# Kernel tuning notes

Hardware: AMD Instinct MI355X
Metric: run time of the kernel (lower is better)

Reference implementation:

```python
import jax, jax.numpy as jnp
import numpy as np

B, N, F = 8, 1024, 256
H, U = 4, 256
NEG = -1e9  # unused (adjacency=None -> full attention)


def setup_inputs() -> dict:
    key = jax.random.key(0)
    k1, k2, k3, k4 = jax.random.split(key, 4)
    x = jax.random.normal(k1, (B, N, F), dtype=jnp.float32)
    # glorot-scale params
    W = jax.random.normal(k2, (H, F, U), dtype=jnp.float32) * (2.0 / (F + U)) ** 0.5
    a_src = jax.random.normal(k3, (H, U, 1), dtype=jnp.float32) * (2.0 / (U + 1)) ** 0.5
    a_dst = jax.random.normal(k4, (H, U, 1), dtype=jnp.float32) * (2.0 / (U + 1)) ** 0.5
    return {"x": x, "W": W, "a_src": a_src, "a_dst": a_dst}


def reference(x, W, a_src, a_dst):
    # per-head linear projection: [B,H,N,U]
    h = jnp.einsum('bnf,hfu->bhnu', x, W)
    # additive attention logits
    src = jnp.einsum('bhnu,hu->bhn', h, a_src[..., 0])  # [B,H,N]
    dst = jnp.einsum('bhnu,hu->bhn', h, a_dst[..., 0])  # [B,H,N]
    scores = src[:, :, :, None] + dst[:, :, None, :]    # [B,H,N,N]
    scores = jax.nn.leaky_relu(scores, negative_slope=0.2)
    attn = jax.nn.softmax(scores, axis=-1)
    h_prime = jnp.einsum('bhnm,bhmu->bhnu', attn, h)    # [B,H,N,U]
    # concat heads: [B,N,H*U]
    return jnp.transpose(h_prime, (0, 2, 1, 3)).reshape(B, N, H * U)
```

## Files before the change

kernel.cpp:

```cpp
#include <hip/hip_runtime.h>
#include <math.h>

constexpr int B_ = 8, N_ = 1024, F_ = 256, H_ = 4, U_ = 256;
constexpr int BH_ = B_ * H_;
constexpr int CH_ = 16;
constexpr int NCH_ = N_ / CH_;
constexpr int M_ = B_ * N_;

typedef short short8 __attribute__((ext_vector_type(8)));
typedef float floatx4 __attribute__((ext_vector_type(4)));

__device__ inline unsigned short f2bf(float f) {
    unsigned u = __float_as_uint(f);
    u += 0x7fff + ((u >> 16) & 1);
    return (unsigned short)(u >> 16);
}
__device__ inline float bf2f(unsigned short s) { return __uint_as_float(((unsigned)s) << 16); }

__device__ inline void gload_lds16(const void* g, void* l) {
    __builtin_amdgcn_global_load_lds(
        (const __attribute__((address_space(1))) void*)g,
        (__attribute__((address_space(3))) void*)(unsigned)(uintptr_t)l,
        16, 0, 0);
}

__global__ __launch_bounds__(256) void prep_w(const float* __restrict__ W,
                                              const float* __restrict__ asr,
                                              const float* __restrict__ ads,
                                              unsigned short* __restrict__ whT,
                                              float* __restrict__ c_src,
                                              float* __restrict__ c_dst) {
    int tid = threadIdx.x;
    if (blockIdx.x < 64) {
        __shared__ float t[64][65];
        int bi = blockIdx.x;
        int f0 = (bi & 3) * 64, u0 = ((bi >> 2) & 3) * 64, h = bi >> 4;
        int c = tid & 63, rbase = tid >> 6;
        #pragma unroll
        for (int rr = 0; rr < 16; ++rr) {
            int r = rr * 4 + rbase;
            t[r][c] = W[((size_t)(h * F_ + f0 + r)) * U_ + u0 + c];
        }
        __syncthreads();
        #pragma unroll
        for (int rr = 0; rr < 16; ++rr) {
            int r = rr * 4 + rbase;
            whT[((size_t)(h * U_ + u0 + r)) * F_ + f0 + c] = f2bf(t[c][r]);
        }
    } else {
        int id = blockIdx.x - 64;
        int h = id >> 2, f0 = (id & 3) * 64;
        int fl = tid >> 2, q = tid & 3;
        int f = f0 + fl;
        const float* Wrow = W + ((size_t)(h * F_ + f)) * U_ + q * 64;
        const float* av = asr + h * U_ + q * 64;
        const float* bv = ads + h * U_ + q * 64;
        float s = 0.f, d = 0.f;
        #pragma unroll
        for (int u = 0; u < 64; ++u) { float ww = Wrow[u]; s += ww * av[u]; d += ww * bv[u]; }
        s += __shfl_xor(s, 1); s += __shfl_xor(s, 2);
        d += __shfl_xor(d, 1); d += __shfl_xor(d, 2);
        if (q == 0) { c_src[h * F_ + f] = s; c_dst[h * F_ + f] = d; }
    }
}

__global__ __launch_bounds__(256) void k1b_fused(const float* __restrict__ x,
                                                 const float* __restrict__ c_src,
                                                 const float* __restrict__ c_dst,
                                                 unsigned short* __restrict__ xh,
                                                 float* __restrict__ srcv,
                                                 float* __restrict__ dstv) {
    int tid = threadIdx.x;
    int lane = tid & 63, w = tid >> 6;
    int row = blockIdx.x * 4 + w;
    int b = row >> 10, n = row & 1023;
    const float4 x4 = *(const float4*)(x + (size_t)row * F_ + lane * 4);
    ushort4 hv;
    hv.x = f2bf(x4.x); hv.y = f2bf(x4.y); hv.z = f2bf(x4.z); hv.w = f2bf(x4.w);
    ((ushort4*)xh)[(size_t)row * (F_ / 4) + lane] = hv;
    #pragma unroll
    for (int hh = 0; hh < H_; ++hh) {
        float4 c4 = *(const float4*)(c_src + hh * F_ + lane * 4);
        float s = x4.x*c4.x + x4.y*c4.y + x4.z*c4.z + x4.w*c4.w;
        #pragma unroll
        for (int off = 32; off; off >>= 1) s += __shfl_xor(s, off);
        float4 d4 = *(const float4*)(c_dst + hh * F_ + lane * 4);
        float d = x4.x*d4.x + x4.y*d4.y + x4.z*d4.z + x4.w*d4.w;
        #pragma unroll
        for (int off = 32; off; off >>= 1) d += __shfl_xor(d, off);
        if (lane == 0) {
            srcv[(size_t)(b * H_ + hh) * N_ + n] = s;
            dstv[(size_t)(b * H_ + hh) * N_ + n] = d;
        }
    }
}

__global__ __launch_bounds__(1024) void k2_all(const float* __restrict__ dstv,
                                               const float* __restrict__ srcv,
                                               float* __restrict__ dvs,
                                               int* __restrict__ invp,
                                               int* __restrict__ spos,
                                               int* __restrict__ srows,
                                               float* __restrict__ se8,
                                               int* __restrict__ cstart) {
    __shared__ float dv[N_];
    __shared__ float keyLA[N_]; __shared__ int idxLA[N_];
    __shared__ float keyLB[N_]; __shared__ int idxLB[N_];
    int bh = blockIdx.x, t = threadIdx.x;

    float ka = dstv[(size_t)bh * N_ + t];  int ia = t;
    float kb = -srcv[(size_t)bh * N_ + t]; int ib = t;

    for (int k = 2; k <= N_; k <<= 1) {
        for (int j = k >> 1; j > 0; j >>= 1) {
            bool up = ((t & k) == 0);
            bool lower = ((t & j) == 0);
            float oa, ob; int oia, oib;
            if (j >= 64) {
                keyLA[t] = ka; idxLA[t] = ia;
                keyLB[t] = kb; idxLB[t] = ib;
                __syncthreads();
                oa = keyLA[t ^ j]; oia = idxLA[t ^ j];
                ob = keyLB[t ^ j]; oib = idxLB[t ^ j];
                __syncthreads();
            } else {
                oa = __shfl_xor(ka, j); oia = __shfl_xor(ia, j);
                ob = __shfl_xor(kb, j); oib = __shfl_xor(ib, j);
            }
            bool swa = up ? (lower ? (ka > oa) : (ka < oa))
                          : (lower ? (ka < oa) : (ka > oa));
            if (swa) { ka = oa; ia = oia; }
            bool swb = up ? (lower ? (kb > ob) : (kb < ob))
                          : (lower ? (kb < ob) : (kb > ob));
            if (swb) { kb = ob; ib = oib; }
        }
    }

    dvs[(size_t)bh * N_ + t] = ka;
    invp[(size_t)bh * N_ + ia] = t;
    dv[t] = ka;
    __syncthreads();

    float s = -kb;
    int lo = 0, hi = N_;
    while (lo < hi) {
        int mid = (lo + hi) >> 1;
        if (dv[mid] <= kb) lo = mid + 1; else hi = mid;
    }
    spos[(size_t)bh * N_ + t] = lo;
    srows[(size_t)bh * N_ + t] = ib;
    se8[(size_t)bh * N_ + t] = expf(0.8f * s);
    idxLA[t] = lo;
    __syncthreads();
    if (t < NCH_ + 1) {
        int target = t * CH_;
        int lo2 = 0, hi2 = N_;
        while (lo2 < hi2) {
            int mid = (lo2 + hi2) >> 1;
            if (idxLA[mid] < target) lo2 = mid + 1; else hi2 = mid;
        }
        cstart[bh * (NCH_ + 1) + t] = lo2;
    }
}

__global__ __launch_bounds__(256) void k1_mfma(const unsigned short* __restrict__ xh,
                                               const unsigned short* __restrict__ whT,
                                               const int* __restrict__ invp,
                                               unsigned short* __restrict__ hbuf) {
    __shared__ __align__(16) unsigned short As[2 * 128 * 64];
    __shared__ int jsL[128];
    unsigned short* Bs = As + 128 * 64;
    const int tid = threadIdx.x;
    const int lane = tid & 63, wv = tid >> 6;
    const int wr = wv >> 1, wc = wv & 1;
    const int m0 = blockIdx.x * 128;
    const int u0 = blockIdx.y * 128;
    const int hh = blockIdx.z;
    const int b = m0 >> 10, n0 = m0 & 1023;
    const int bh = b * H_ + hh;

    floatx4 acc[4][4] = {};

    const char* Asrc = (const char*)xh;
    const char* Bsrc = (const char*)(whT + (size_t)hh * U_ * F_);

    const int ch_row = lane >> 3;
    const int ch_col = (lane & 7) * 16;

    for (int t = 0; t < 4; ++t) {
        const size_t kb = (size_t)t * 128;
        #pragma unroll
        for (int i = 0; i < 4; ++i) {
            int c = wv * 4 + i;
            int row = c * 8 + ch_row;
            gload_lds16(Asrc + (size_t)(m0 + row) * 512 + kb + ch_col,
                        (char*)As + c * 1024);
            gload_lds16(Bsrc + (size_t)(u0 + row) * 512 + kb + ch_col,
                        (char*)Bs + c * 1024);
        }
        __syncthreads();
        #pragma unroll
        for (int ks = 0; ks < 2; ++ks) {
            short8 af[4], bfr[4];
            #pragma unroll
            for (int mf = 0; mf < 4; ++mf) {
                int row = wr * 64 + mf * 16 + (lane & 15);
                af[mf] = *(const short8*)&As[row * 64 + ks * 32 + (lane >> 4) * 8];
            }
            #pragma unroll
            for (int nf = 0; nf < 4; ++nf) {
                int row = wc * 64 + nf * 16 + (lane & 15);
                bfr[nf] = *(const short8*)&Bs[row * 64 + ks * 32 + (lane >> 4) * 8];
            }
            #pragma unroll
            for (int mf = 0; mf < 4; ++mf)
                #pragma unroll
                for (int nf = 0; nf < 4; ++nf)
                    acc[mf][nf] = __builtin_amdgcn_mfma_f32_16x16x32_bf16(
                        af[mf], bfr[nf], acc[mf][nf], 0, 0, 0);
        }
        __syncthreads();
    }

    unsigned short* S = As;
    const int rquad = (lane >> 4) * 4;
    const int ucol = lane & 15;
    #pragma unroll
    for (int mf = 0; mf < 4; ++mf)
        #pragma unroll
        for (int j = 0; j < 4; ++j) {
            int rloc = wr * 64 + mf * 16 + rquad + j;
            #pragma unroll
            for (int nf = 0; nf < 4; ++nf)
                S[rloc * 128 + wc * 64 + nf * 16 + ucol] = f2bf(acc[mf][nf][j]);
        }
    if (tid < 128) jsL[tid] = invp[(size_t)bh * N_ + n0 + tid];
    __syncthreads();
    #pragma unroll
    for (int i = 0; i < 8; ++i) {
        int flat = tid + i * 256;
        int rloc = flat >> 4, slot = flat & 15;
        short8 v = *(const short8*)&S[rloc * 128 + slot * 8];
        *(short8*)&hbuf[((size_t)bh * N_ + jsL[rloc]) * U_ + u0 + slot * 8] = v;
    }
}

__global__ __launch_bounds__(256) void k3a_partial(const unsigned short* __restrict__ hbuf,
                                                   const float* __restrict__ dvs,
                                                   float* __restrict__ cT1, float* __restrict__ cT2,
                                                   float* __restrict__ cZ1, float* __restrict__ cZ2) {
    __shared__ float w1s[CH_], w2s[CH_];
    __shared__ floatx4 A1s[4][64], A2s[4][64];
    int bh = blockIdx.x / NCH_, c = blockIdx.x % NCH_;
    int tid = threadIdx.x, w = tid >> 6, l = tid & 63;
    const ushort4* hb4 = (const ushort4*)(hbuf + ((size_t)bh * N_ + c * CH_) * U_);
    ushort4 h0 = hb4[(4 * w + 0) * 64 + l];
    ushort4 h1 = hb4[(4 * w + 1) * 64 + l];
    ushort4 h2 = hb4[(4 * w + 2) * 64 + l];
    ushort4 h3 = hb4[(4 * w + 3) * 64 + l];
    floatx4 v0 = {bf2f(h0.x), bf2f(h0.y), bf2f(h0.z), bf2f(h0.w)};
    floatx4 v1 = {bf2f(h1.x), bf2f(h1.y), bf2f(h1.z), bf2f(h1.w)};
    floatx4 v2 = {bf2f(h2.x), bf2f(h2.y), bf2f(h2.z), bf2f(h2.w)};
    floatx4 v3 = {bf2f(h3.x), bf2f(h3.y), bf2f(h3.z), bf2f(h3.w)};
    if (tid < CH_) {
        float vv = dvs[(size_t)bh * N_ + c * CH_ + tid];
        w1s[tid] = expf(vv);
        w2s[tid] = expf(0.2f * vv);
    }
    __syncthreads();
    floatx4 s1 = w1s[4*w]*v0 + w1s[4*w+1]*v1 + w1s[4*w+2]*v2 + w1s[4*w+3]*v3;
    floatx4 s2 = w2s[4*w]*v0 + w2s[4*w+1]*v1 + w2s[4*w+2]*v2 + w2s[4*w+3]*v3;
    A1s[w][l] = s1; A2s[w][l] = s2;
    __syncthreads();
    if (tid < 64) {
        floatx4 r1 = A1s[0][tid] + A1s[1][tid] + A1s[2][tid] + A1s[3][tid];
        floatx4 r2 = A2s[0][tid] + A2s[1][tid] + A2s[2][tid] + A2s[3][tid];
        ((floatx4*)(cT1 + (size_t)(bh * NCH_ + c) * U_))[tid] = r1;
        ((floatx4*)(cT2 + (size_t)(bh * NCH_ + c) * U_))[tid] = r2;
    }
    if (tid == 0) {
        float z1 = 0.f, z2 = 0.f;
        #pragma unroll
        for (int r = 0; r < CH_; ++r) { z1 += w1s[r]; z2 += w2s[r]; }
        cZ1[bh * NCH_ + c] = z1; cZ2[bh * NCH_ + c] = z2;
    }
}

__global__ __launch_bounds__(256) void k3b_combine(const float* __restrict__ cT1, const float* __restrict__ cT2,
                                                   const float* __restrict__ cZ1, const float* __restrict__ cZ2,
                                                   float* __restrict__ b1, float* __restrict__ b2,
                                                   float* __restrict__ bz1, float* __restrict__ bz2) {
    int bh = blockIdx.x;
    int u = threadIdx.x;
    float v[NCH_];
    #pragma unroll
    for (int c = 0; c < NCH_; ++c) v[c] = cT2[(size_t)(bh * NCH_ + c) * U_ + u];
    float acc2 = 0.f;
    #pragma unroll
    for (int c = 0; c < NCH_; ++c) {
        b2[(size_t)(bh * NCH_ + c) * U_ + u] = acc2;
        acc2 += v[c];
    }
    #pragma unroll
    for (int c = 0; c < NCH_; ++c) v[c] = cT1[(size_t)(bh * NCH_ + c) * U_ + u];
    float acc1 = 0.f;
    #pragma unroll
    for (int c = NCH_ - 1; c >= 0; --c) {
        b1[(size_t)(bh * NCH_ + c) * U_ + u] = acc1;
        acc1 += v[c];
    }
    if (u < NCH_) {
        float z1 = cZ1[bh * NCH_ + u];
        float z2 = cZ2[bh * NCH_ + u];
        float i1 = z1, i2 = z2;
        #pragma unroll
        for (int off = 1; off < NCH_; off <<= 1) {
            float t1 = __shfl_up(i1, off, 64);
            float t2 = __shfl_up(i2, off, 64);
            if (u >= off) { i1 += t1; i2 += t2; }
        }
        float tot1 = __shfl(i1, NCH_ - 1, 64);
        bz1[bh * NCH_ + u] = tot1 - i1;
        bz2[bh * NCH_ + u] = i2 - z2;
    }
}

__global__ __launch_bounds__(256) void k3cd_emit(const unsigned short* __restrict__ hbuf,
                                                 const float* __restrict__ dvs,
                                                 const float* __restrict__ b1, const float* __restrict__ b2,
                                                 const float* __restrict__ bz1, const float* __restrict__ bz2,
                                                 const int* __restrict__ spos,
                                                 const int* __restrict__ srows,
                                                 const float* __restrict__ se8,
                                                 const int* __restrict__ cstart,
                                                 float* __restrict__ out) {
    __shared__ floatx4 P1s[CH_ + 1][64];
    __shared__ floatx4 P2s[CH_ + 1][64];
    __shared__ floatx4 T1s[4][64], T2s[4][64];
    __shared__ float w1s[CH_], w2s[CH_];
    __shared__ float zx1[CH_ + 1], zx2[CH_ + 1];
    __shared__ int sps[256], srs[256];
    __shared__ float s8s[256];

    int bh = blockIdx.x / NCH_, c = blockIdx.x % NCH_;
    int tid = threadIdx.x, w = tid >> 6, l = tid & 63;
    int b = bh >> 2, hh = bh & 3;

    const ushort4* hb4 = (const ushort4*)(hbuf + ((size_t)bh * N_ + c * CH_) * U_);
    ushort4 h0 = hb4[(4 * w + 0) * 64 + l];
    ushort4 h1 = hb4[(4 * w + 1) * 64 + l];
    ushort4 h2 = hb4[(4 * w + 2) * 64 + l];
    ushort4 h3 = hb4[(4 * w + 3) * 64 + l];
    floatx4 v0 = {bf2f(h0.x), bf2f(h0.y), bf2f(h0.z), bf2f(h0.w)};
    floatx4 v1 = {bf2f(h1.x), bf2f(h1.y), bf2f(h1.z), bf2f(h1.w)};
    floatx4 v2 = {bf2f(h2.x), bf2f(h2.y), bf2f(h2.z), bf2f(h2.w)};
    floatx4 v3 = {bf2f(h3.x), bf2f(h3.y), bf2f(h3.z), bf2f(h3.w)};
    if (tid < CH_) {
        float vv = dvs[(size_t)bh * N_ + c * CH_ + tid];
        w1s[tid] = expf(vv);
        w2s[tid] = expf(0.2f * vv);
    }
    __syncthreads();
    float a0 = w1s[4*w], a1 = w1s[4*w+1], a2 = w1s[4*w+2], a3 = w1s[4*w+3];
    float c0 = w2s[4*w], c1 = w2s[4*w+1], c2 = w2s[4*w+2], c3 = w2s[4*w+3];
    floatx4 q1_1 = a0 * v0;
    floatx4 q1_2 = q1_1 + a1 * v1;
    floatx4 q1_3 = q1_2 + a2 * v2;
    floatx4 tw1  = q1_3 + a3 * v3;
    floatx4 q2_1 = c0 * v0;
    floatx4 q2_2 = q2_1 + c1 * v1;
    floatx4 q2_3 = q2_2 + c2 * v2;
    floatx4 tw2  = q2_3 + c3 * v3;
    T1s[w][l] = tw1; T2s[w][l] = tw2;
    if (tid == 0) {
        float z1 = 0.f, z2 = 0.f;
        #pragma unroll
        for (int r = 0; r < CH_; ++r) { zx1[r] = z1; zx2[r] = z2; z1 += w1s[r]; z2 += w2s[r]; }
        zx1[CH_] = z1; zx2[CH_] = z2;
    }
    __syncthreads();
    floatx4 base1 = {0.f, 0.f, 0.f, 0.f}, base2 = {0.f, 0.f, 0.f, 0.f};
    if (w > 0) { base1 += T1s[0][l]; base2 += T2s[0][l]; }
    if (w > 1) { base1 += T1s[1][l]; base2 += T2s[1][l]; }
    if (w > 2) { base1 += T1s[2][l]; base2 += T2s[2][l]; }
    P1s[4*w+0][l] = base1;         P2s[4*w+0][l] = base2;
    P1s[4*w+1][l] = base1 + q1_1;  P2s[4*w+1][l] = base2 + q2_1;
    P1s[4*w+2][l] = base1 + q1_2;  P2s[4*w+2][l] = base2 + q2_2;
    P1s[4*w+3][l] = base1 + q1_3;  P2s[4*w+3][l] = base2 + q2_3;
    if (w == 3) { P1s[CH_][l] = base1 + tw1; P2s[CH_][l] = base2 + tw2; }
    __syncthreads();

    floatx4 t1 = P1s[CH_][l];
    float tz1 = zx1[CH_];
    floatx4 b1u = ((const floatx4*)(b1 + (size_t)(bh * NCH_ + c) * U_))[l];
    floatx4 b2u = ((const floatx4*)(b2 + (size_t)(bh * NCH_ + c) * U_))[l];
    float bz1c = bz1[bh * NCH_ + c], bz2c = bz2[bh * NCH_ + c];

    const int*   spos_b  = spos  + (size_t)bh * N_;
    const int*   srows_b = srows + (size_t)bh * N_;
    const float* se8_b   = se8   + (size_t)bh * N_;
    const int j0 = cstart[bh * (NCH_ + 1) + c];
    const int e0 = (c == NCH_ - 1) ? N_ : cstart[bh * (NCH_ + 1) + c + 1];

    for (int t0 = j0; t0 < e0; t0 += 256) {
        int jj = t0 + tid;
        if (jj < e0) { sps[tid] = spos_b[jj]; srs[tid] = srows_b[jj]; s8s[tid] = se8_b[jj]; }
        __syncthreads();
        int cnt = min(256, e0 - t0);
        for (int k = w; k < cnt; k += 4) {
            int   rr  = sps[k] - c * CH_;
            int   row = srs[k];
            float e8  = s8s[k];
            floatx4 s1 = b1u + (t1 - P1s[rr][l]);
            floatx4 s2 = b2u + P2s[rr][l];
            float den = e8 * (bz1c + (tz1 - zx1[rr])) + (bz2c + zx2[rr]);
            float rden = 1.0f / den;
            floatx4 o = (e8 * s1 + s2) * rden;
            *(floatx4*)(out + ((size_t)(b * N_ + row)) * (H_ * U_) + hh * U_ + 4 * l) = o;
        }
        __syncthreads();
    }
}

extern "C" void kernel_launch(void* const* d_in, const int* in_sizes, int n_in,
                              void* d_out, int out_size, void* d_ws, size_t ws_size,
                              hipStream_t stream) {
    const float* x    = (const float*)d_in[0];
    const float* W    = (const float*)d_in[1];
    const float* asr  = (const float*)d_in[2];
    const float* ads  = (const float*)d_in[3];
    float* out = (float*)d_out;

    char* ws = (char*)d_ws;
    size_t off = 0;
    auto alloc = [&](size_t nfloats) -> float* {
        float* p = (float*)(ws + off);
        off += ((nfloats * 4 + 255) / 256) * 256;
        return p;
    };
    unsigned short* hbuf = (unsigned short*)alloc((size_t)BH_ * N_ * U_ / 2);
    float* srcv  = alloc((size_t)BH_ * N_);
    float* dstv  = alloc((size_t)BH_ * N_);
    float* c_src = alloc(H_ * F_);
    float* c_dst = alloc(H_ * F_);
    float* dvs   = alloc((size_t)BH_ * N_);
    int*   invp  = (int*)alloc((size_t)BH_ * N_);
    int*   srows = (int*)alloc((size_t)BH_ * N_);
    int*   spos  = (int*)alloc((size_t)BH_ * N_);
    float* se8   = alloc((size_t)BH_ * N_);
    int*   cstart= (int*)alloc(BH_ * (NCH_ + 1));
    float* cT1   = alloc((size_t)BH_ * NCH_ * U_);
    float* cT2   = alloc((size_t)BH_ * NCH_ * U_);
    float* cZ1   = alloc(BH_ * NCH_);
    float* cZ2   = alloc(BH_ * NCH_);
    float* b1    = alloc((size_t)BH_ * NCH_ * U_);
    float* b2    = alloc((size_t)BH_ * NCH_ * U_);
    float* bz1   = alloc(BH_ * NCH_);
    float* bz2   = alloc(BH_ * NCH_);
    unsigned short* xh  = (unsigned short*)alloc((size_t)M_ * F_ / 2);
    unsigned short* whT = (unsigned short*)alloc((size_t)H_ * U_ * F_ / 2);
    (void)ws_size; (void)in_sizes; (void)n_in; (void)out_size;

    prep_w<<<80, 256, 0, stream>>>(W, asr, ads, whT, c_src, c_dst);
    k1b_fused<<<(B_ * N_) / 4, 256, 0, stream>>>(x, c_src, c_dst, xh, srcv, dstv);
    k2_all<<<BH_, 1024, 0, stream>>>(dstv, srcv, dvs, invp, spos, srows, se8, cstart);
    k1_mfma<<<dim3(M_ / 128, U_ / 128, H_), 256, 0, stream>>>(xh, whT, invp, hbuf);
    k3a_partial<<<BH_ * NCH_, 256, 0, stream>>>(hbuf, dvs, cT1, cT2, cZ1, cZ2);
    k3b_combine<<<BH_, 256, 0, stream>>>(cT1, cT2, cZ1, cZ2, b1, b2, bz1, bz2);
    k3cd_emit<<<BH_ * NCH_, 256, 0, stream>>>(hbuf, dvs, b1, b2, bz1, bz2,
                                              spos, srows, se8, cstart, out);
}
```

Measured before the change: 82.71 us.

## Fuse three-stage chunked prefix-scan attention into one per-head kernel

Replaces the partial-sum, combine and emit kernels (plus cstart computation in the sort kernel) with a single kernel where each block handles one batch-head and a 64-column slice. Eight segments of 128 rows compute segment totals, combine them through LDS, then rescan their rows while emitting outputs for the sorted source positions. This removes two launches and the global round-trips of per-chunk partial sums. The trade-off is far fewer blocks (128 of 512 threads), serial per-thread loops over 128 rows, scalar 2-byte loads, and possible load imbalance when many sources fall in one segment.

After: 114.0 us. 37.8% more time.

```diff
diff --git a/kernel.cpp b/kernel.cpp
--- a/kernel.cpp
+++ b/kernel.cpp
@@ -3,8 +3,6 @@
 
 constexpr int B_ = 8, N_ = 1024, F_ = 256, H_ = 4, U_ = 256;
 constexpr int BH_ = B_ * H_;
-constexpr int CH_ = 16;
-constexpr int NCH_ = N_ / CH_;
 constexpr int M_ = B_ * N_;
 
 typedef short short8 __attribute__((ext_vector_type(8)));
@@ -101,8 +99,7 @@
                                                int* __restrict__ invp,
                                                int* __restrict__ spos,
                                                int* __restrict__ srows,
-                                               float* __restrict__ se8,
-                                               int* __restrict__ cstart) {
+                                               float* __restrict__ se8) {
     __shared__ float dv[N_];
     __shared__ float keyLA[N_]; __shared__ int idxLA[N_];
     __shared__ float keyLB[N_]; __shared__ int idxLB[N_];
@@ -150,17 +147,6 @@
     spos[(size_t)bh * N_ + t] = lo;
     srows[(size_t)bh * N_ + t] = ib;
     se8[(size_t)bh * N_ + t] = expf(0.8f * s);
-    idxLA[t] = lo;
-    __syncthreads();
-    if (t < NCH_ + 1) {
-        int target = t * CH_;
-        int lo2 = 0, hi2 = N_;
-        while (lo2 < hi2) {
-            int mid = (lo2 + hi2) >> 1;
-            if (idxLA[mid] < target) lo2 = mid + 1; else hi2 = mid;
-        }
-        cstart[bh * (NCH_ + 1) + t] = lo2;
-    }
 }
 
 __global__ __launch_bounds__(256) void k1_mfma(const unsigned short* __restrict__ xh,
@@ -178,6 +164,8 @@
     const int hh = blockIdx.z;
     const int b = m0 >> 10, n0 = m0 & 1023;
     const int bh = b * H_ + hh;
+
+    if (tid < 128) jsL[tid] = invp[(size_t)bh * N_ + n0 + tid];
 
     floatx4 acc[4][4] = {};
 
@@ -234,7 +222,6 @@
             for (int nf = 0; nf < 4; ++nf)
                 S[rloc * 128 + wc * 64 + nf * 16 + ucol] = f2bf(acc[mf][nf][j]);
         }
-    if (tid < 128) jsL[tid] = invp[(size_t)bh * N_ + n0 + tid];
     __syncthreads();
     #pragma unroll
     for (int i = 0; i < 8; ++i) {
@@ -245,180 +232,110 @@
     }
 }
 
-__global__ __launch_bounds__(256) void k3a_partial(const unsigned short* __restrict__ hbuf,
-                                                   const float* __restrict__ dvs,
-                                                   float* __restrict__ cT1, float* __restrict__ cT2,
-                                                   float* __restrict__ cZ1, float* __restrict__ cZ2) {
-    __shared__ float w1s[CH_], w2s[CH_];
-    __shared__ floatx4 A1s[4][64], A2s[4][64];
-    int bh = blockIdx.x / NCH_, c = blockIdx.x % NCH_;
-    int tid = threadIdx.x, w = tid >> 6, l = tid & 63;
-    const ushort4* hb4 = (const ushort4*)(hbuf + ((size_t)bh * N_ + c * CH_) * U_);
-    ushort4 h0 = hb4[(4 * w + 0) * 64 + l];
-    ushort4 h1 = hb4[(4 * w + 1) * 64 + l];
-    ushort4 h2 = hb4[(4 * w + 2) * 64 + l];
-    ushort4 h3 = hb4[(4 * w + 3) * 64 + l];
-    floatx4 v0 = {bf2f(h0.x), bf2f(h0.y), bf2f(h0.z), bf2f(h0.w)};
-    floatx4 v1 = {bf2f(h1.x), bf2f(h1.y), bf2f(h1.z), bf2f(h1.w)};
-    floatx4 v2 = {bf2f(h2.x), bf2f(h2.y), bf2f(h2.z), bf2f(h2.w)};
-    floatx4 v3 = {bf2f(h3.x), bf2f(h3.y), bf2f(h3.z), bf2f(h3.w)};
-    if (tid < CH_) {
-        float vv = dvs[(size_t)bh * N_ + c * CH_ + tid];
-        w1s[tid] = expf(vv);
-        w2s[tid] = expf(0.2f * vv);
+__global__ __launch_bounds__(512) void k3_fused(const unsigned short* __restrict__ hbuf,
+                                                const float* __restrict__ dvs,
+                                                const int* __restrict__ spos,
+                                                const int* __restrict__ srows,
+                                                const float* __restrict__ se8,
+                                                float* __restrict__ out) {
+    __shared__ float w1s[N_], w2s[N_];
+    __shared__ int   sposL[N_], srowsL[N_];
+    __shared__ float se8L[N_];
+    __shared__ float t1L[8][64], t2L[8][64];
+    __shared__ float zt1L[8], zt2L[8];
+
+    const int blk = blockIdx.x;
+    const int bh = blk >> 2, slice = blk & 3;
+    const int tid = threadIdx.x;
+    const int lane = tid & 63, seg = tid >> 6;
+    const int b = bh >> 2, hh = bh & 3;
+
+    for (int i = tid; i < N_; i += 512) {
+        float vv = dvs[(size_t)bh * N_ + i];
+        w1s[i] = expf(vv);
+        w2s[i] = expf(0.2f * vv);
+        sposL[i]  = spos[(size_t)bh * N_ + i];
+        srowsL[i] = srows[(size_t)bh * N_ + i];
+        se8L[i]   = se8[(size_t)bh * N_ + i];
     }
     __syncthreads();
-    floatx4 s1 = w1s[4*w]*v0 + w1s[4*w+1]*v1 + w1s[4*w+2]*v2 + w1s[4*w+3]*v3;
-    floatx4 s2 = w2s[4*w]*v0 + w2s[4*w+1]*v1 + w2s[4*w+2]*v2 + w2s[4*w+3]*v3;
-    A1s[w][l] = s1; A2s[w][l] = s2;
+
+    const unsigned short* hbp =
+        hbuf + ((size_t)bh * N_ + seg * 128) * U_ + slice * 64 + lane;
+
+    float t1 = 0.f, t2 = 0.f;
+    #pragma unroll 16
+    for (int r = 0; r < 128; ++r) {
+        float v = bf2f(hbp[(size_t)r * U_]);
+        t1 += w1s[seg * 128 + r] * v;
+        t2 += w2s[seg * 128 + r] * v;
+    }
+    t1L[seg][lane] = t1; t2L[seg][lane] = t2;
+    float zz1 = 0.f, zz2 = 0.f;
+    for (int r = lane; r < 128; r += 64) {
+        zz1 += w1s[seg * 128 + r];
+        zz2 += w2s[seg * 128 + r];
+    }
+    #pragma unroll
+    for (int off = 32; off; off >>= 1) {
+        zz1 += __shfl_xor(zz1, off);
+        zz2 += __shfl_xor(zz2, off);
+    }
+    if (lane == 0) { zt1L[seg] = zz1; zt2L[seg] = zz2; }
     __syncthreads();
-    if (tid < 64) {
-        floatx4 r1 = A1s[0][tid] + A1s[1][tid] + A1s[2][tid] + A1s[3][tid];
-        floatx4 r2 = A2s[0][tid] + A2s[1][tid] + A2s[2][tid] + A2s[3][tid];
-        ((floatx4*)(cT1 + (size_t)(bh * NCH_ + c) * U_))[tid] = r1;
-        ((floatx4*)(cT2 + (size_t)(bh * NCH_ + c) * U_))[tid] = r2;
-    }
-    if (tid == 0) {
-        float z1 = 0.f, z2 = 0.f;
-        #pragma unroll
-        for (int r = 0; r < CH_; ++r) { z1 += w1s[r]; z2 += w2s[r]; }
-        cZ1[bh * NCH_ + c] = z1; cZ2[bh * NCH_ + c] = z2;
-    }
-}
-
-__global__ __launch_bounds__(256) void k3b_combine(const float* __restrict__ cT1, const float* __restrict__ cT2,
-                                                   const float* __restrict__ cZ1, const float* __restrict__ cZ2,
-                                                   float* __restrict__ b1, float* __restrict__ b2,
-                                                   float* __restrict__ bz1, float* __restrict__ bz2) {
-    int bh = blockIdx.x;
-    int u = threadIdx.x;
-    float v[NCH_];
-    #pragma unroll
-    for (int c = 0; c < NCH_; ++c) v[c] = cT2[(size_t)(bh * NCH_ + c) * U_ + u];
-    float acc2 = 0.f;
-    #pragma unroll
-    for (int c = 0; c < NCH_; ++c) {
-        b2[(size_t)(bh * NCH_ + c) * U_ + u] = acc2;
-        acc2 += v[c];
-    }
-    #pragma unroll
-    for (int c = 0; c < NCH_; ++c) v[c] = cT1[(size_t)(bh * NCH_ + c) * U_ + u];
-    float acc1 = 0.f;
-    #pragma unroll
-    for (int c = NCH_ - 1; c >= 0; --c) {
-        b1[(size_t)(bh * NCH_ + c) * U_ + u] = acc1;
-        acc1 += v[c];
-    }
-    if (u < NCH_) {
-        float z1 = cZ1[bh * NCH_ + u];
-        float z2 = cZ2[bh * NCH_ + u];
-        float i1 = z1, i2 = z2;
-        #pragma unroll
-        for (int off = 1; off < NCH_; off <<= 1) {
-            float t1 = __shfl_up(i1, off, 64);
-            float t2 = __shfl_up(i2, off, 64);
-            if (u >= off) { i1 += t1; i2 += t2; }
-        }
-        float tot1 = __shfl(i1, NCH_ - 1, 64);
-        bz1[bh * NCH_ + u] = tot1 - i1;
-        bz2[bh * NCH_ + u] = i2 - z2;
-    }
-}
-
-__global__ __launch_bounds__(256) void k3cd_emit(const unsigned short* __restrict__ hbuf,
-                                                 const float* __restrict__ dvs,
-                                                 const float* __restrict__ b1, const float* __restrict__ b2,
-                                                 const float* __restrict__ bz1, const float* __restrict__ bz2,
-                                                 const int* __restrict__ spos,
-                                                 const int* __restrict__ srows,
-                                                 const float* __restrict__ se8,
-                                                 const int* __restrict__ cstart,
-                                                 float* __restrict__ out) {
-    __shared__ floatx4 P1s[CH_ + 1][64];
-    __shared__ floatx4 P2s[CH_ + 1][64];
-    __shared__ floatx4 T1s[4][64], T2s[4][64];
-    __shared__ float w1s[CH_], w2s[CH_];
-    __shared__ float zx1[CH_ + 1], zx2[CH_ + 1];
-    __shared__ int sps[256], srs[256];
-    __shared__ float s8s[256];
-
-    int bh = blockIdx.x / NCH_, c = blockIdx.x % NCH_;
-    int tid = threadIdx.x, w = tid >> 6, l = tid & 63;
-    int b = bh >> 2, hh = bh & 3;
-
-    const ushort4* hb4 = (const ushort4*)(hbuf + ((size_t)bh * N_ + c * CH_) * U_);
-    ushort4 h0 = hb4[(4 * w + 0) * 64 + l];
-    ushort4 h1 = hb4[(4 * w + 1) * 64 + l];
-    ushort4 h2 = hb4[(4 * w + 2) * 64 + l];
-    ushort4 h3 = hb4[(4 * w + 3) * 64 + l];
-    floatx4 v0 = {bf2f(h0.x), bf2f(h0.y), bf2f(h0.z), bf2f(h0.w)};
-    floatx4 v1 = {bf2f(h1.x), bf2f(h1.y), bf2f(h1.z), bf2f(h1.w)};
-    floatx4 v2 = {bf2f(h2.x), bf2f(h2.y), bf2f(h2.z), bf2f(h2.w)};
-    floatx4 v3 = {bf2f(h3.x), bf2f(h3.y), bf2f(h3.z), bf2f(h3.w)};
-    if (tid < CH_) {
-        float vv = dvs[(size_t)bh * N_ + c * CH_ + tid];
-        w1s[tid] = expf(vv);
-        w2s[tid] = expf(0.2f * vv);
-    }
-    __syncthreads();
-    float a0 = w1s[4*w], a1 = w1s[4*w+1], a2 = w1s[4*w+2], a3 = w1s[4*w+3];
-    float c0 = w2s[4*w], c1 = w2s[4*w+1], c2 = w2s[4*w+2], c3 = w2s[4*w+3];
-    floatx4 q1_1 = a0 * v0;
-    floatx4 q1_2 = q1_1 + a1 * v1;
-    floatx4 q1_3 = q1_2 + a2 * v2;
-    floatx4 tw1  = q1_3 + a3 * v3;
-    floatx4 q2_1 = c0 * v0;
-    floatx4 q2_2 = q2_1 + c1 * v1;
-    floatx4 q2_3 = q2_2 + c2 * v2;
-    floatx4 tw2  = q2_3 + c3 * v3;
-    T1s[w][l] = tw1; T2s[w][l] = tw2;
-    if (tid == 0) {
-        float z1 = 0.f, z2 = 0.f;
-        #pragma unroll
-        for (int r = 0; r < CH_; ++r) { zx1[r] = z1; zx2[r] = z2; z1 += w1s[r]; z2 += w2s[r]; }
-        zx1[CH_] = z1; zx2[CH_] = z2;
-    }
-    __syncthreads();
-    floatx4 base1 = {0.f, 0.f, 0.f, 0.f}, base2 = {0.f, 0.f, 0.f, 0.f};
-    if (w > 0) { base1 += T1s[0][l]; base2 += T2s[0][l]; }
-    if (w > 1) { base1 += T1s[1][l]; base2 += T2s[1][l]; }
-    if (w > 2) { base1 += T1s[2][l]; base2 += T2s[2][l]; }
-    P1s[4*w+0][l] = base1;         P2s[4*w+0][l] = base2;
-    P1s[4*w+1][l] = base1 + q1_1;  P2s[4*w+1][l] = base2 + q2_1;
-    P1s[4*w+2][l] = base1 + q1_2;  P2s[4*w+2][l] = base2 + q2_2;
-    P1s[4*w+3][l] = base1 + q1_3;  P2s[4*w+3][l] = base2 + q2_3;
-    if (w == 3) { P1s[CH_][l] = base1 + tw1; P2s[CH_][l] = base2 + tw2; }
-    __syncthreads();
-
-    floatx4 t1 = P1s[CH_][l];
-    float tz1 = zx1[CH_];
-    floatx4 b1u = ((const floatx4*)(b1 + (size_t)(bh * NCH_ + c) * U_))[l];
-    floatx4 b2u = ((const floatx4*)(b2 + (size_t)(bh * NCH_ + c) * U_))[l];
-    float bz1c = bz1[bh * NCH_ + c], bz2c = bz2[bh * NCH_ + c];
-
-    const int*   spos_b  = spos  + (size_t)bh * N_;
-    const int*   srows_b = srows + (size_t)bh * N_;
-    const float* se8_b   = se8   + (size_t)bh * N_;
-    const int j0 = cstart[bh * (NCH_ + 1) + c];
-    const int e0 = (c == NCH_ - 1) ? N_ : cstart[bh * (NCH_ + 1) + c + 1];
-
-    for (int t0 = j0; t0 < e0; t0 += 256) {
-        int jj = t0 + tid;
-        if (jj < e0) { sps[tid] = spos_b[jj]; srs[tid] = srows_b[jj]; s8s[tid] = se8_b[jj]; }
-        __syncthreads();
-        int cnt = min(256, e0 - t0);
-        for (int k = w; k < cnt; k += 4) {
-            int   rr  = sps[k] - c * CH_;
-            int   row = srs[k];
-            float e8  = s8s[k];
-            floatx4 s1 = b1u + (t1 - P1s[rr][l]);
-            floatx4 s2 = b2u + P2s[rr][l];
-            float den = e8 * (bz1c + (tz1 - zx1[rr])) + (bz2c + zx2[rr]);
-            float rden = 1.0f / den;
-            floatx4 o = (e8 * s1 + s2) * rden;
-            *(floatx4*)(out + ((size_t)(b * N_ + row)) * (H_ * U_) + hh * U_ + 4 * l) = o;
-        }
-        __syncthreads();
+
+    float T1 = 0.f, pre1 = 0.f, pre2 = 0.f;
+    float Tz1 = 0.f, prez1 = 0.f, prez2 = 0.f;
+    #pragma unroll
+    for (int ss = 0; ss < 8; ++ss) {
+        float a1 = t1L[ss][lane], a2 = t2L[ss][lane];
+        T1 += a1; Tz1 += zt1L[ss];
+        if (ss < seg) { pre1 += a1; pre2 += a2; prez1 += zt1L[ss]; prez2 += zt2L[ss]; }
+    }
+
+    int lo = 0, hi = N_;
+    const int startp = seg * 128;
+    while (lo < hi) { int m = (lo + hi) >> 1; if (sposL[m] < startp) lo = m + 1; else hi = m; }
+    int j = lo;
+    lo = j; hi = N_;
+    const int endp = startp + 128;
+    while (lo < hi) { int m = (lo + hi) >> 1; if (sposL[m] < endp) lo = m + 1; else hi = m; }
+    const int e = lo;
+
+    float p1 = 0.f, p2 = 0.f, pz1 = 0.f, pz2 = 0.f;
+    for (int rt = 0; rt < 128; rt += 16) {
+        float vv[16];
+        #pragma unroll
+        for (int q = 0; q < 16; ++q) vv[q] = bf2f(hbp[(size_t)(rt + q) * U_]);
+        #pragma unroll
+        for (int q = 0; q < 16; ++q) {
+            int row = startp + rt + q;
+            while (j < e && sposL[j] == row) {
+                float e8 = se8L[j];
+                int   srow = srowsL[j];
+                float s1 = T1 - (pre1 + p1);
+                float s2 = pre2 + p2;
+                float den = e8 * (Tz1 - (prez1 + pz1)) + (prez2 + pz2);
+                out[((size_t)(b * N_ + srow)) * (H_ * U_) + hh * U_ + slice * 64 + lane]
+                    = (e8 * s1 + s2) / den;
+                ++j;
+            }
+            float w1 = w1s[row], w2 = w2s[row];
+            p1 += w1 * vv[q]; p2 += w2 * vv[q];
+            pz1 += w1;        pz2 += w2;
+        }
+    }
+    if (seg == 7) {
+        while (j < N_) {
+            float e8 = se8L[j];
+            int   srow = srowsL[j];
+            float s1 = T1 - (pre1 + p1);
+            float s2 = pre2 + p2;
+            float den = e8 * (Tz1 - (prez1 + pz1)) + (prez2 + pz2);
+            out[((size_t)(b * N_ + srow)) * (H_ * U_) + hh * U_ + slice * 64 + lane]
+                = (e8 * s1 + s2) / den;
+            ++j;
+        }
     }
 }
 
@@ -448,25 +365,13 @@
     int*   srows = (int*)alloc((size_t)BH_ * N_);
     int*   spos  = (int*)alloc((size_t)BH_ * N_);
     float* se8   = alloc((size_t)BH_ * N_);
-    int*   cstart= (int*)alloc(BH_ * (NCH_ + 1));
-    float* cT1   = alloc((size_t)BH_ * NCH_ * U_);
-    float* cT2   = alloc((size_t)BH_ * NCH_ * U_);
-    float* cZ1   = alloc(BH_ * NCH_);
-    float* cZ2   = alloc(BH_ * NCH_);
-    float* b1    = alloc((size_t)BH_ * NCH_ * U_);
-    float* b2    = alloc((size_t)BH_ * NCH_ * U_);
-    float* bz1   = alloc(BH_ * NCH_);
-    float* bz2   = alloc(BH_ * NCH_);
     unsigned short* xh  = (unsigned short*)alloc((size_t)M_ * F_ / 2);
     unsigned short* whT = (unsigned short*)alloc((size_t)H_ * U_ * F_ / 2);
     (void)ws_size; (void)in_sizes; (void)n_in; (void)out_size;
 
     prep_w<<<80, 256, 0, stream>>>(W, asr, ads, whT, c_src, c_dst);
     k1b_fused<<<(B_ * N_) / 4, 256, 0, stream>>>(x, c_src, c_dst, xh, srcv, dstv);
-    k2_all<<<BH_, 1024, 0, stream>>>(dstv, srcv, dvs, invp, spos, srows, se8, cstart);
+    k2_all<<<BH_, 1024, 0, stream>>>(dstv, srcv, dvs, invp, spos, srows, se8);
     k1_mfma<<<dim3(M_ / 128, U_ / 128, H_), 256, 0, stream>>>(xh, whT, invp, hbuf);
-    k3a_partial<<<BH_ * NCH_, 256, 0, stream>>>(hbuf, dvs, cT1, cT2, cZ1, cZ2);
-    k3b_combine<<<BH_, 256, 0, stream>>>(cT1, cT2, cZ1, cZ2, b1, b2, bz1, bz2);
-    k3cd_emit<<<BH_ * NCH_, 256, 0, stream>>>(hbuf, dvs, b1, b2, bz1, bz2,
-                                              spos, srows, se8, cstart, out);
-}
+    k3_fused<<<BH_ * 4, 512, 0, stream>>>(hbuf, dvs, spos, srows, se8, out);
+}
```
